# Kernel optimization log

Measured on AMD Instinct MI355X. Metric: run time of the kernel, lower is better.

Reference implementation:

```python
import jax, jax.numpy as jnp
import numpy as np

D_MODEL = 1024
N_HEADS = 16
D_HEAD = D_MODEL // N_HEADS
HIDDEN = 4 * D_MODEL
EPS = 1e-5
ROPE_BASE = 10000.0


def layernorm(x, g, b):
    mu = jnp.mean(x, axis=-1, keepdims=True)
    var = jnp.mean((x - mu) ** 2, axis=-1, keepdims=True)
    return (x - mu) * jax.lax.rsqrt(var + EPS) * g + b


def rope(t, pos):
    # t: (B, N, D), pos: (N,) int -> rotary transform over D (half-split pairs)
    half = t.shape[-1] // 2
    inv_freq = 1.0 / (ROPE_BASE ** (jnp.arange(half, dtype=jnp.float32) / half))
    ang = pos.astype(jnp.float32)[:, None] * inv_freq  # (N, half)
    cos, sin = jnp.cos(ang), jnp.sin(ang)
    t1, t2 = t[..., :half], t[..., half:]
    return jnp.concatenate([t1 * cos - t2 * sin, t1 * sin + t2 * cos], axis=-1)


def setup_inputs() -> dict:
    key = jax.random.key(0)
    ks = jax.random.split(key, 12)
    B, N, D, H = 2, 2048, D_MODEL, HIDDEN
    s = 0.02
    return {
        "x": jax.random.normal(ks[0], (B, N, D), jnp.float32),
        "pos": jnp.arange(N, dtype=jnp.int32),
        "Wq": jax.random.normal(ks[1], (D, D), jnp.float32) * s,
        "bq": jnp.zeros((D,), jnp.float32),
        "Wk": jax.random.normal(ks[2], (D, D), jnp.float32) * s,
        "bk": jnp.zeros((D,), jnp.float32),
        "Wv": jax.random.normal(ks[3], (D, D), jnp.float32) * s,
        "bv": jnp.zeros((D,), jnp.float32),
        "Wo": jax.random.normal(ks[4], (D, D), jnp.float32) * s,
        "bo": jnp.zeros((D,), jnp.float32),
        "g1": jnp.ones((D,), jnp.float32),
        "b1": jnp.zeros((D,), jnp.float32),
        "g2": jnp.ones((D,), jnp.float32),
        "b2": jnp.zeros((D,), jnp.float32),
        "W1": jax.random.normal(ks[5], (D, H), jnp.float32) * s,
        "bm1": jnp.zeros((H,), jnp.float32),
        "W2": jax.random.normal(ks[6], (H, D), jnp.float32) * s,
        "bm2": jnp.zeros((D,), jnp.float32),
    }


def reference(x, pos, Wq, bq, Wk, bk, Wv, bv, Wo, bo, g1, b1, g2, b2, W1, bm1, W2, bm2):
    B, N, D = x.shape
    Hh, dh = N_HEADS, D_HEAD

    # --- attention sublayer (pre-norm) ---
    h = layernorm(x, g1, b1)
    q = h @ Wq + bq
    k = h @ Wk + bk
    v = h @ Wv + bv
    q = rope(q, pos)
    k = rope(k, pos)
    # split heads: (B, Hh, N, dh)
    q = q.reshape(B, N, Hh, dh).transpose(0, 2, 1, 3)
    k = k.reshape(B, N, Hh, dh).transpose(0, 2, 1, 3)
    v = v.reshape(B, N, Hh, dh).transpose(0, 2, 1, 3)
    scores = jnp.einsum("bhqd,bhkd->bhqk", q, k) / jnp.sqrt(jnp.float32(dh))
    attn = jax.nn.softmax(scores, axis=-1)
    ctx = jnp.einsum("bhqk,bhkd->bhqd", attn, v)
    ctx = ctx.transpose(0, 2, 1, 3).reshape(B, N, D)
    x = x + ctx @ Wo + bo

    # --- MLP sublayer (pre-norm, exact GELU) ---
    h = layernorm(x, g2, b2)
    h = jax.nn.gelu(h @ W1 + bm1, approximate=False)
    x = x + h @ W2 + bm2
    return x
```

## Files before the change

### kernel.cpp

```cpp
#include <hip/hip_runtime.h>

typedef __bf16 bf16x8 __attribute__((ext_vector_type(8)));
typedef __bf16 bf16x4 __attribute__((ext_vector_type(4)));
typedef float  f32x4  __attribute__((ext_vector_type(4)));

#define D_MODEL 1024
#define SEQ     2048
#define BATCH   2
#define NH      16
#define DH      64
#define HID     4096
#define ROWS    (BATCH*SEQ)

static __device__ __forceinline__ void gl_lds16(const __bf16* g, __bf16* l) {
  __builtin_amdgcn_global_load_lds(
      (const __attribute__((address_space(1))) unsigned int*)g,
      (__attribute__((address_space(3))) unsigned int*)l, 16, 0, 0);
}

__global__ __launch_bounds__(256) void ln_kernel(
    const float* __restrict__ x, const float* __restrict__ g,
    const float* __restrict__ b, __bf16* __restrict__ out)
{
  int row = blockIdx.x;
  const float* xr = x + (size_t)row * D_MODEL;
  int i0 = threadIdx.x * 4;
  f32x4 xv = *(const f32x4*)(xr + i0);
  float s  = xv[0] + xv[1] + xv[2] + xv[3];
  float ss = xv[0]*xv[0] + xv[1]*xv[1] + xv[2]*xv[2] + xv[3]*xv[3];
#pragma unroll
  for (int off = 1; off < 64; off <<= 1) {
    s  += __shfl_xor(s,  off, 64);
    ss += __shfl_xor(ss, off, 64);
  }
  __shared__ float red[8];
  int wave = threadIdx.x >> 6;
  if ((threadIdx.x & 63) == 0) { red[wave] = s; red[4 + wave] = ss; }
  __syncthreads();
  s  = red[0] + red[1] + red[2] + red[3];
  ss = red[4] + red[5] + red[6] + red[7];
  float mu  = s * (1.0f / D_MODEL);
  float var = ss * (1.0f / D_MODEL) - mu * mu;
  float inv = rsqrtf(var + 1e-5f);
  f32x4 gv = *(const f32x4*)(g + i0);
  f32x4 bv = *(const f32x4*)(b + i0);
  bf16x4 ov;
#pragma unroll
  for (int j = 0; j < 4; ++j)
    ov[j] = (__bf16)((xv[j] - mu) * inv * gv[j] + bv[j]);
  *(bf16x4*)(out + (size_t)row * D_MODEL + i0) = ov;
}

__global__ __launch_bounds__(256) void convT_kernel(
    const float* __restrict__ W, __bf16* __restrict__ Wt, int K, int N)
{
  __shared__ float T[32][33];
  int n0 = blockIdx.x * 32, k0 = blockIdx.y * 32;
  int r  = threadIdx.x >> 3;
  int c4 = (threadIdx.x & 7) * 4;
  f32x4 v = *(const f32x4*)(W + (size_t)(k0 + r) * N + n0 + c4);
#pragma unroll
  for (int i = 0; i < 4; ++i) T[r][c4 + i] = v[i];
  __syncthreads();
  bf16x4 o;
#pragma unroll
  for (int i = 0; i < 4; ++i) o[i] = (__bf16)T[c4 + i][r];
  *(bf16x4*)(Wt + (size_t)(n0 + r) * K + k0 + c4) = o;
}

__global__ void biascat_kernel(const float* __restrict__ a,
                               const float* __restrict__ b,
                               const float* __restrict__ c,
                               float* __restrict__ o)
{
  int i = blockIdx.x * 256 + threadIdx.x;
  o[i] = i < 1024 ? a[i] : (i < 2048 ? b[i - 1024] : c[i - 2048]);
}

__global__ __launch_bounds__(512, 2) void gemm256(
    const __bf16* __restrict__ A, const __bf16* __restrict__ Bt,
    const float* __restrict__ bias, const float* __restrict__ resid,
    void* __restrict__ Cv, int M, int N, int K, int act, int c_fp32)
{
  __shared__ __bf16 As[2][256 * 64];
  __shared__ __bf16 Bs[2][256 * 64];
  int tid = threadIdx.x, lane = tid & 63, wv = tid >> 6;
  int quad = lane >> 4, l16 = lane & 15;
  int wr = wv >> 2, wc = wv & 3;
  int gx = M >> 8, gy = N >> 8;
  int nwg = gx * gy;
  int xcd = blockIdx.x & 7;
  int q = nwg >> 3, r8 = nwg & 7;
  int wg = (xcd < r8 ? xcd * (q + 1) : r8 * (q + 1) + (xcd - r8) * q) + (blockIdx.x >> 3);
  int row0 = (wg % gx) << 8;
  int col0 = (wg / gx) << 8;
  int s_r  = lane >> 3;
  int s_src = ((lane & 7) ^ s_r) * 8;
  int sw = l16 & 7;
  int NT = K >> 6;
  f32x4 acc[8][4] = {};

#define G256_STAGE(kt, b)                                                     \
  {                                                                           \
    int k0_ = (kt) * 64;                                                      \
    _Pragma("unroll")                                                         \
    for (int rd = 0; rd < 4; ++rd) {                                          \
      int rrow = rd * 64 + wv * 8 + s_r;                                      \
      gl_lds16(A  + (size_t)(row0 + rrow) * K + k0_ + s_src,                  \
               &As[b][rd * 4096 + wv * 512]);                                 \
      gl_lds16(Bt + (size_t)(col0 + rrow) * K + k0_ + s_src,                  \
               &Bs[b][rd * 4096 + wv * 512]);                                 \
    }                                                                         \
  }

  G256_STAGE(0, 0);
  G256_STAGE(1, 1);

  for (int t = 0; t < NT; ++t) {
    if (t + 1 < NT) asm volatile("s_waitcnt vmcnt(8)" ::: "memory");
    else            asm volatile("s_waitcnt vmcnt(0)" ::: "memory");
    __builtin_amdgcn_s_barrier();
    const __bf16* Ab = &As[t & 1][0];
    const __bf16* Bb = &Bs[t & 1][0];
    __builtin_amdgcn_s_setprio(1);
#pragma unroll
    for (int kk = 0; kk < 2; ++kk) {
      int slot = ((kk * 4 + quad) ^ sw) * 8;
      bf16x8 bfr[4];
#pragma unroll
      for (int j = 0; j < 4; ++j)
        bfr[j] = *(const bf16x8*)(Bb + (wc * 64 + j * 16 + l16) * 64 + slot);
      bf16x8 afr[8];
#pragma unroll
      for (int i = 0; i < 8; ++i)
        afr[i] = *(const bf16x8*)(Ab + (wr * 128 + i * 16 + l16) * 64 + slot);
#pragma unroll
      for (int i = 0; i < 8; ++i)
#pragma unroll
        for (int j = 0; j < 4; ++j)
          acc[i][j] = __builtin_amdgcn_mfma_f32_16x16x32_bf16(afr[i], bfr[j], acc[i][j], 0, 0, 0);
    }
    __builtin_amdgcn_s_setprio(0);
    __builtin_amdgcn_s_barrier();
    if (t + 2 < NT) G256_STAGE(t + 2, t & 1);
  }

#pragma unroll
  for (int i = 0; i < 8; ++i) {
    int grow = row0 + wr * 128 + i * 16 + quad * 4;
#pragma unroll
    for (int j = 0; j < 4; ++j) {
      int gcol = col0 + wc * 64 + j * 16 + l16;
      float bsv = bias[gcol];
#pragma unroll
      for (int r = 0; r < 4; ++r) {
        size_t off = (size_t)(grow + r) * N + gcol;
        float v = acc[i][j][r] + bsv;
        if (act) v = 0.5f * v * (1.0f + erff(v * 0.70710678118654752f));
        if (resid) v += resid[off];
        if (c_fp32) ((float*)Cv)[off] = v;
        else        ((__bf16*)Cv)[off] = (__bf16)v;
      }
    }
  }
}

__global__ __launch_bounds__(256) void gemm128(
    const __bf16* __restrict__ A, const __bf16* __restrict__ Bt,
    const float* __restrict__ bias, const float* __restrict__ resid,
    void* __restrict__ Cv, int M, int N, int K, int act, int c_fp32)
{
  __shared__ __bf16 As[128 * 64];
  __shared__ __bf16 Bs[128 * 64];
  int tid = threadIdx.x, lane = tid & 63, wv = tid >> 6;
  int quad = lane >> 4, l16 = lane & 15;
  int wr = wv >> 1, wc = wv & 1;
  int gx = M >> 7, gy = N >> 7;
  int blk = blockIdx.x;
  int xcd = blk & 7, t = blk >> 3;
  int row0 = (t % gx) * 128;
  int col0 = (xcd * (gy >> 3) + t / gx) * 128;
  int s_r8 = lane >> 3;
  int s_c8 = lane & 7;
  int s_src = (s_c8 ^ s_r8) * 8;
  int sw = l16 & 7;
  f32x4 acc[4][4] = {};

  for (int k0 = 0; k0 < K; k0 += 64) {
#pragma unroll
    for (int p = 0; p < 4; ++p) {
      int r = p * 32 + wv * 8 + s_r8;
      gl_lds16(A  + (size_t)(row0 + r) * K + k0 + s_src, As + p * 2048 + wv * 512);
      gl_lds16(Bt + (size_t)(col0 + r) * K + k0 + s_src, Bs + p * 2048 + wv * 512);
    }
    __syncthreads();
#pragma unroll
    for (int kk = 0; kk < 2; ++kk) {
      int slot = ((kk * 4 + quad) ^ sw) * 8;
      bf16x8 af[4], bf[4];
#pragma unroll
      for (int i = 0; i < 4; ++i) {
        af[i] = *(const bf16x8*)(As + (wr * 64 + i * 16 + l16) * 64 + slot);
        bf[i] = *(const bf16x8*)(Bs + (wc * 64 + i * 16 + l16) * 64 + slot);
      }
#pragma unroll
      for (int i = 0; i < 4; ++i)
#pragma unroll
        for (int j = 0; j < 4; ++j)
          acc[i][j] = __builtin_amdgcn_mfma_f32_16x16x32_bf16(af[i], bf[j], acc[i][j], 0, 0, 0);
    }
    __syncthreads();
  }
#pragma unroll
  for (int i = 0; i < 4; ++i) {
    int grow = row0 + wr * 64 + i * 16 + quad * 4;
#pragma unroll
    for (int j = 0; j < 4; ++j) {
      int gcol = col0 + wc * 64 + j * 16 + l16;
      float bsv = bias[gcol];
#pragma unroll
      for (int r = 0; r < 4; ++r) {
        size_t off = (size_t)(grow + r) * N + gcol;
        float v = acc[i][j][r] + bsv;
        if (act) v = 0.5f * v * (1.0f + erff(v * 0.70710678118654752f));
        if (resid) v += resid[off];
        if (c_fp32) ((float*)Cv)[off] = v;
        else        ((__bf16*)Cv)[off] = (__bf16)v;
      }
    }
  }
}

__global__ __launch_bounds__(256) void gemm64x128(
    const __bf16* __restrict__ A, const __bf16* __restrict__ Bt,
    const float* __restrict__ bias, const float* __restrict__ resid,
    void* __restrict__ Cv, int M, int N, int K, int act, int c_fp32)
{
  __shared__ __bf16 As[2][64 * 64];
  __shared__ __bf16 Bs[2][128 * 64];
  int tid = threadIdx.x, lane = tid & 63, wv = tid >> 6;
  int quad = lane >> 4, l16 = lane & 15;
  int wr = wv >> 1, wc = wv & 1;
  int gx = M >> 6, gy = N >> 7;
  int blk = blockIdx.x;
  int xcd = blk & 7, t = blk >> 3;
  int row0 = (t % gx) * 64;
  int col0 = (xcd * (gy >> 3) + t / gx) * 128;
  int s_r8 = lane >> 3;
  int s_c8 = lane & 7;
  int s_src = (s_c8 ^ s_r8) * 8;
  int sw = l16 & 7;
  int NT = K >> 6;
  f32x4 acc[2][4] = {};

#define G64_STAGE(kt, b)                                                      \
  {                                                                           \
    int k0_ = (kt) * 64;                                                      \
    _Pragma("unroll")                                                         \
    for (int p = 0; p < 4; ++p) {                                             \
      int r = p * 32 + wv * 8 + s_r8;                                         \
      if (p < 2)                                                              \
        gl_lds16(A + (size_t)(row0 + r) * K + k0_ + s_src,                    \
                 &As[b][p * 2048 + wv * 512]);                                \
      gl_lds16(Bt + (size_t)(col0 + r) * K + k0_ + s_src,                     \
               &Bs[b][p * 2048 + wv * 512]);                                  \
    }                                                                         \
  }

  G64_STAGE(0, 0);
  G64_STAGE(1, 1);

  for (int tt = 0; tt < NT; ++tt) {
    if (tt + 1 < NT) asm volatile("s_waitcnt vmcnt(6)" ::: "memory");
    else             asm volatile("s_waitcnt vmcnt(0)" ::: "memory");
    __builtin_amdgcn_s_barrier();
    const __bf16* Ab = &As[tt & 1][0];
    const __bf16* Bb = &Bs[tt & 1][0];
    __builtin_amdgcn_s_setprio(1);
#pragma unroll
    for (int kk = 0; kk < 2; ++kk) {
      int slot = ((kk * 4 + quad) ^ sw) * 8;
      bf16x8 af[2], bf[4];
#pragma unroll
      for (int i = 0; i < 2; ++i)
        af[i] = *(const bf16x8*)(Ab + (wr * 32 + i * 16 + l16) * 64 + slot);
#pragma unroll
      for (int j = 0; j < 4; ++j)
        bf[j] = *(const bf16x8*)(Bb + (wc * 64 + j * 16 + l16) * 64 + slot);
#pragma unroll
      for (int i = 0; i < 2; ++i)
#pragma unroll
        for (int j = 0; j < 4; ++j)
          acc[i][j] = __builtin_amdgcn_mfma_f32_16x16x32_bf16(af[i], bf[j], acc[i][j], 0, 0, 0);
    }
    __builtin_amdgcn_s_setprio(0);
    __builtin_amdgcn_s_barrier();
    if (tt + 2 < NT) G64_STAGE(tt + 2, tt & 1);
  }

#pragma unroll
  for (int i = 0; i < 2; ++i) {
    int grow = row0 + wr * 32 + i * 16 + quad * 4;
#pragma unroll
    for (int j = 0; j < 4; ++j) {
      int gcol = col0 + wc * 64 + j * 16 + l16;
      float bsv = bias[gcol];
#pragma unroll
      for (int r = 0; r < 4; ++r) {
        size_t off = (size_t)(grow + r) * N + gcol;
        float v = acc[i][j][r] + bsv;
        if (act) v = 0.5f * v * (1.0f + erff(v * 0.70710678118654752f));
        if (resid) v += resid[off];
        if (c_fp32) ((float*)Cv)[off] = v;
        else        ((__bf16*)Cv)[off] = (__bf16)v;
      }
    }
  }
}

__global__ __launch_bounds__(256) void rope_repack(
    const __bf16* __restrict__ qkv, const int* __restrict__ pos,
    __bf16* __restrict__ Qh, __bf16* __restrict__ Kh)
{
  int row = blockIdx.x;
  int b = row >> 11, n = row & (SEQ - 1);
  float p = (float)pos[n];
  const __bf16* qr = qkv + (size_t)row * 3072;
#pragma unroll
  for (int t = 0; t < 2; ++t) {
    int i = threadIdx.x + t * 256;
    float fr  = expf(-9.210340371976184f * ((float)i * (1.0f / 512.0f)));
    float ang = p * fr;
    float sn, c;
    sincosf(ang, &sn, &c);
    float q1 = (float)qr[i],        q2 = (float)qr[512 + i];
    float k1 = (float)qr[1024 + i], k2 = (float)qr[1536 + i];
    int h1 = i >> 6, d1 = i & 63;
    int h2 = (i + 512) >> 6;
    size_t o1 = ((size_t)(b * NH + h1) * SEQ + n) * DH + d1;
    size_t o2 = ((size_t)(b * NH + h2) * SEQ + n) * DH + d1;
    Qh[o1] = (__bf16)((q1 * c - q2 * sn) * 0.125f);
    Qh[o2] = (__bf16)((q1 * sn + q2 * c) * 0.125f);
    Kh[o1] = (__bf16)(k1 * c - k2 * sn);
    Kh[o2] = (__bf16)(k1 * sn + k2 * c);
  }
}

__global__ __launch_bounds__(256) void vtrans_kernel(
    const __bf16* __restrict__ Vsrc, int vstride, __bf16* __restrict__ Vt,
    int blocked)
{
  __shared__ __bf16 T[64][72];
  int bh = blockIdx.x;
  int kb = blockIdx.y * 64;
  int b = bh >> 4, h = bh & 15;
  int tid = threadIdx.x;
#pragma unroll
  for (int t = 0; t < 2; ++t) {
    int u = tid + t * 256;
    int r = u >> 3, seg = (u & 7) * 8;
    bf16x8 v = *(const bf16x8*)(Vsrc + (size_t)(b * SEQ + kb + r) * vstride + h * DH + seg);
    *(bf16x8*)(&T[r][seg]) = v;
  }
  __syncthreads();
#pragma unroll
  for (int t = 0; t < 2; ++t) {
    int u = tid + t * 256;
    int d = u >> 3, ks = (u & 7) * 8;
    bf16x8 o;
#pragma unroll
    for (int i = 0; i < 8; ++i) o[i] = T[ks + i][d];
    if (blocked) {
      int key = kb + ks;
      *(bf16x8*)(Vt + (((size_t)bh * (SEQ / 128) + (key >> 7)) * DH + d) * 128 + (key & 127)) = o;
    } else {
      *(bf16x8*)(Vt + ((size_t)bh * DH + d) * SEQ + kb + ks) = o;
    }
  }
}

#define KS 136
__global__ __launch_bounds__(256) void attn_split(
    const __bf16* __restrict__ Qh, const __bf16* __restrict__ Kh,
    const __bf16* __restrict__ Vt, __bf16* __restrict__ pacc,
    float* __restrict__ pml)
{
  __shared__ __bf16 Ks[128 * 64];
  __shared__ __bf16 Vs[64 * 128];
  __shared__ __bf16 Pl[4][16 * KS];
  int tid = threadIdx.x, lane = tid & 63, wave = tid >> 6;
  int quad = lane >> 4, l16 = lane & 15;
  int blk = blockIdx.x;
  int split = blk >> 10;
  int rr = blk & 1023;
  int bh  = ((rr & 7) << 2) | ((rr >> 3) & 3);
  int q64 = rr >> 5;
  int q0 = q64 * 64 + wave * 16;
  const __bf16* qbase = Qh + (size_t)bh * SEQ * DH;
  const __bf16* kbase = Kh + (size_t)bh * SEQ * DH;
  const __bf16* vbase = Vt + (size_t)bh * SEQ * DH;
  const __bf16* qp = qbase + (size_t)(q0 + l16) * DH + quad * 8;
  bf16x8 qf0 = *(const bf16x8*)(qp);
  bf16x8 qf1 = *(const bf16x8*)(qp + 32);
  float lrow[4] = {0.f, 0.f, 0.f, 0.f};
  f32x4 acc[4] = {};
  __bf16* pw = &Pl[wave][0];
  int s_kr = lane >> 3;
  int s_k8 = lane & 7;
  int s_vd = lane >> 4;
  int s_vs = lane & 15;
  int sw8  = l16 & 7;

  int kb0 = split * (SEQ / 2);
  for (int it = 0; it < (SEQ / 2) / 128; ++it) {
    int kb = kb0 + it * 128;
    const __bf16* kt = kbase + (size_t)kb * DH;
    const __bf16* vt = vbase + (size_t)(kb >> 7) * (DH * 128);
    __syncthreads();
#pragma unroll
    for (int p = 0; p < 4; ++p) {
      int key0 = p * 32 + wave * 8;
      int swz  = (key0 >> 3) & 7;
      gl_lds16(kt + (key0 + s_kr) * DH + ((s_k8 ^ swz) * 8), Ks + p * 2048 + wave * 512);
      int d = p * 16 + wave * 4 + s_vd;
      gl_lds16(vt + d * 128 + ((s_vs ^ (d & 15)) * 8), Vs + p * 2048 + wave * 512);
    }
    __syncthreads();
    f32x4 s[8];
#pragma unroll
    for (int j = 0; j < 8; ++j) {
      const __bf16* kr = Ks + (l16 * 8 + j) * 64;
      bf16x8 kf0 = *(const bf16x8*)(kr + (quad ^ sw8) * 8);
      bf16x8 kf1 = *(const bf16x8*)(kr + ((quad ^ sw8) ^ 4) * 8);
      f32x4 z = {};
      z = __builtin_amdgcn_mfma_f32_16x16x32_bf16(qf0, kf0, z, 0, 0, 0);
      s[j] = __builtin_amdgcn_mfma_f32_16x16x32_bf16(qf1, kf1, z, 0, 0, 0);
    }
#pragma unroll
    for (int r = 0; r < 4; ++r) {
      bf16x8 pv;
      float rs = 0.f;
#pragma unroll
      for (int j = 0; j < 8; ++j) {
        float pj = __expf(s[j][r]);
        rs += pj;
        pv[j] = (__bf16)pj;
      }
      lrow[r] += rs;
      *(bf16x8*)(pw + (quad * 4 + r) * KS + l16 * 8) = pv;
    }
#pragma unroll
    for (int kk = 0; kk < 4; ++kk) {
      bf16x8 pf = *(const bf16x8*)(pw + l16 * KS + kk * 32 + quad * 8);
#pragma unroll
      for (int j = 0; j < 4; ++j) {
        int d = j * 16 + l16;
        bf16x8 vf = *(const bf16x8*)(Vs + d * 128 + (((kk * 4 + quad) ^ (d & 15)) * 8));
        acc[j] = __builtin_amdgcn_mfma_f32_16x16x32_bf16(pf, vf, acc[j], 0, 0, 0);
      }
    }
  }
#pragma unroll
  for (int r = 0; r < 4; ++r)
#pragma unroll
    for (int off = 1; off < 16; off <<= 1) lrow[r] += __shfl_xor(lrow[r], off, 64);
#pragma unroll
  for (int r = 0; r < 4; ++r) {
    int brow = wave * 16 + quad * 4 + r;
#pragma unroll
    for (int j = 0; j < 4; ++j)
      pacc[((size_t)blk * 64 + brow) * 64 + j * 16 + l16] = (__bf16)acc[j][r];
    if (l16 == 0) {
      pml[(size_t)blk * 128 + brow]      = 0.f;
      pml[(size_t)blk * 128 + 64 + brow] = lrow[r];
    }
  }
}

__global__ __launch_bounds__(256) void attn_combine(
    const __bf16* __restrict__ pacc, const float* __restrict__ pml,
    __bf16* __restrict__ ctx)
{
  int bq = blockIdx.x;
  int q64 = bq & 31, bh = bq >> 5;
  int b = bh >> 4, h = bh & 15;
  int tid = threadIdx.x;
  int r = tid >> 2;
  int c = (tid & 3) * 16;
  int blk0 = ((q64 * 4 + (bh & 3)) << 3) | (bh >> 2);
  int blk1 = blk0 + 1024;
  float m0 = pml[(size_t)blk0 * 128 + r], l0 = pml[(size_t)blk0 * 128 + 64 + r];
  float m1 = pml[(size_t)blk1 * 128 + r], l1 = pml[(size_t)blk1 * 128 + 64 + r];
  float m = fmaxf(m0, m1);
  float w0 = __expf(m0 - m), w1 = __expf(m1 - m);
  float inv = 1.0f / (w0 * l0 + w1 * l1);
  size_t r0 = ((size_t)blk0 * 64 + r) * 64 + c;
  size_t r1 = ((size_t)blk1 * 64 + r) * 64 + c;
  size_t ob = ((size_t)(b * SEQ) + q64 * 64 + r) * D_MODEL + h * DH + c;
#pragma unroll
  for (int g = 0; g < 2; ++g) {
    bf16x8 a0 = *(const bf16x8*)(pacc + r0 + g * 8);
    bf16x8 a1 = *(const bf16x8*)(pacc + r1 + g * 8);
    bf16x8 o;
#pragma unroll
    for (int i = 0; i < 8; ++i)
      o[i] = (__bf16)((w0 * (float)a0[i] + w1 * (float)a1[i]) * inv);
    *(bf16x8*)(ctx + ob + g * 8) = o;
  }
}

__global__ __launch_bounds__(256) void rope_inplace(
    __bf16* __restrict__ ql, __bf16* __restrict__ kl,
    const int* __restrict__ pos, int stride)
{
  int row = blockIdx.x;
  int n = row & (SEQ - 1);
  float p = (float)pos[n];
  const size_t rbase = (size_t)row * stride;
#pragma unroll
  for (int t = 0; t < 2; ++t) {
    int i = threadIdx.x + t * 256;
    float fr  = expf(-9.210340371976184f * ((float)i * (1.0f / 512.0f)));
    float ang = p * fr;
    float sn, c;
    sincosf(ang, &sn, &c);
    float q1 = (float)ql[rbase + i], q2 = (float)ql[rbase + 512 + i];
    float k1 = (float)kl[rbase + i], k2 = (float)kl[rbase + 512 + i];
    ql[rbase + i]       = (__bf16)(q1 * c - q2 * sn);
    ql[rbase + 512 + i] = (__bf16)(q1 * sn + q2 * c);
    kl[rbase + i]       = (__bf16)(k1 * c - k2 * sn);
    kl[rbase + 512 + i] = (__bf16)(k1 * sn + k2 * c);
  }
}

__global__ __launch_bounds__(256) void attn_kernel(
    const __bf16* __restrict__ Q, const __bf16* __restrict__ K,
    const __bf16* __restrict__ Vt, __bf16* __restrict__ ctx, int qkstride)
{
  __shared__ __bf16 Pl[4][16 * KS];
  int tid = threadIdx.x, lane = tid & 63, wave = tid >> 6;
  int quad = lane >> 4, l16 = lane & 15;
  int blk = blockIdx.x;
  int q64 = blk & 31;
  int bh  = blk >> 5;
  int b = bh >> 4, h = bh & 15;
  int q0 = q64 * 64 + wave * 16;
  const __bf16* qbase = Q + (size_t)b * SEQ * qkstride + h * DH;
  const __bf16* kbase = K + (size_t)b * SEQ * qkstride + h * DH;
  const __bf16* vbase = Vt + (size_t)bh * DH * SEQ;
  const __bf16* qp = qbase + (size_t)(q0 + l16) * qkstride + quad * 8;
  bf16x8 qf0 = *(const bf16x8*)(qp);
  bf16x8 qf1 = *(const bf16x8*)(qp + 32);
  float mrow[4] = {-1e30f, -1e30f, -1e30f, -1e30f};
  float lrow[4] = {0.f, 0.f, 0.f, 0.f};
  f32x4 acc[4] = {};
  __bf16* pw = &Pl[wave][0];

  for (int kb = 0; kb < SEQ; kb += 128) {
    f32x4 s[8];
#pragma unroll
    for (int j = 0; j < 8; ++j) {
      const __bf16* kp = kbase + (size_t)(kb + l16 * 8 + j) * qkstride + quad * 8;
      bf16x8 kf0 = *(const bf16x8*)(kp);
      bf16x8 kf1 = *(const bf16x8*)(kp + 32);
      f32x4 z = {};
      z = __builtin_amdgcn_mfma_f32_16x16x32_bf16(qf0, kf0, z, 0, 0, 0);
      z = __builtin_amdgcn_mfma_f32_16x16x32_bf16(qf1, kf1, z, 0, 0, 0);
#pragma unroll
      for (int r = 0; r < 4; ++r) s[j][r] = z[r] * 0.125f;
    }
#pragma unroll
    for (int r = 0; r < 4; ++r) {
      float mx = s[0][r];
#pragma unroll
      for (int j = 1; j < 8; ++j) mx = fmaxf(mx, s[j][r]);
#pragma unroll
      for (int off = 1; off < 16; off <<= 1) mx = fmaxf(mx, __shfl_xor(mx, off, 64));
      float mn = fmaxf(mrow[r], mx);
      float al = __expf(mrow[r] - mn);
      float p[8], rs = 0.f;
#pragma unroll
      for (int j = 0; j < 8; ++j) { p[j] = __expf(s[j][r] - mn); rs += p[j]; }
#pragma unroll
      for (int off = 1; off < 16; off <<= 1) rs += __shfl_xor(rs, off, 64);
      lrow[r] = lrow[r] * al + rs;
      mrow[r] = mn;
#pragma unroll
      for (int j = 0; j < 4; ++j) acc[j][r] *= al;
      bf16x8 pv;
#pragma unroll
      for (int j = 0; j < 8; ++j) pv[j] = (__bf16)p[j];
      *(bf16x8*)(pw + (quad * 4 + r) * KS + l16 * 8) = pv;
    }
#pragma unroll
    for (int kk = 0; kk < 4; ++kk) {
      bf16x8 pf = *(const bf16x8*)(pw + l16 * KS + kk * 32 + quad * 8);
#pragma unroll
      for (int j = 0; j < 4; ++j) {
        bf16x8 vf = *(const bf16x8*)(vbase + (size_t)(j * 16 + l16) * SEQ + kb + kk * 32 + quad * 8);
        acc[j] = __builtin_amdgcn_mfma_f32_16x16x32_bf16(pf, vf, acc[j], 0, 0, 0);
      }
    }
  }
#pragma unroll
  for (int r = 0; r < 4; ++r) {
    int row = q0 + quad * 4 + r;
    float inv = 1.0f / lrow[r];
    size_t obase = ((size_t)(b * SEQ) + row) * D_MODEL + h * DH;
#pragma unroll
    for (int j = 0; j < 4; ++j)
      ctx[obase + j * 16 + l16] = (__bf16)(acc[j][r] * inv);
  }
}

extern "C" void kernel_launch(void* const* d_in, const int* in_sizes, int n_in,
                              void* d_out, int out_size, void* d_ws, size_t ws_size,
                              hipStream_t stream)
{
  const float* x   = (const float*)d_in[0];
  const int*   pos = (const int*)  d_in[1];
  const float* Wq  = (const float*)d_in[2];
  const float* bq  = (const float*)d_in[3];
  const float* Wk  = (const float*)d_in[4];
  const float* bk  = (const float*)d_in[5];
  const float* Wv  = (const float*)d_in[6];
  const float* bv  = (const float*)d_in[7];
  const float* Wo  = (const float*)d_in[8];
  const float* bo  = (const float*)d_in[9];
  const float* g1  = (const float*)d_in[10];
  const float* b1  = (const float*)d_in[11];
  const float* g2  = (const float*)d_in[12];
  const float* b2  = (const float*)d_in[13];
  const float* W1  = (const float*)d_in[14];
  const float* bm1 = (const float*)d_in[15];
  const float* W2  = (const float*)d_in[16];
  const float* bm2 = (const float*)d_in[17];
  float* out = (float*)d_out;

  const size_t MB = 1024 * 1024;
  char* w = (char*)d_ws;
  dim3 blk(256);
  dim3 blk512(512);
  dim3 gConvD(D_MODEL / 32, D_MODEL / 32);
  dim3 gConv1(HID / 32, D_MODEL / 32);
  dim3 gConv2(D_MODEL / 32, HID / 32);
  dim3 gVt(BATCH * NH, SEQ / 64);

  if (ws_size >= (size_t)96 * MB) {
    __bf16* hln   = (__bf16*)(w + 0 * MB);
    float*  x1    = (float*) (w + 8 * MB);
    __bf16* qkv   = (__bf16*)(w + 24 * MB);
    __bf16* pacc  = (__bf16*)(w + 24 * MB);
    float*  pml   = (float*) (w + 41 * MB);
    __bf16* hmlp  = (__bf16*)(w + 24 * MB);
    __bf16* Qh    = (__bf16*)(w + 48 * MB);
    __bf16* ctx   = (__bf16*)(w + 48 * MB);
    __bf16* Kh    = (__bf16*)(w + 56 * MB);
    __bf16* W2T   = (__bf16*)(w + 56 * MB);
    __bf16* Vt    = (__bf16*)(w + 64 * MB);
    __bf16* W1T   = (__bf16*)(w + 64 * MB);
    __bf16* WqkvT = (__bf16*)(w + 72 * MB);
    __bf16* WoT   = (__bf16*)(w + 78 * MB);
    float*  bqkv  = (float*) (w + 80 * MB);

    convT_kernel<<<gConvD, blk, 0, stream>>>(Wq, WqkvT,               D_MODEL, D_MODEL);
    convT_kernel<<<gConvD, blk, 0, stream>>>(Wk, WqkvT + 1024 * 1024, D_MODEL, D_MODEL);
    convT_kernel<<<gConvD, blk, 0, stream>>>(Wv, WqkvT + 2048 * 1024, D_MODEL, D_MODEL);
    convT_kernel<<<gConvD, blk, 0, stream>>>(Wo, WoT, D_MODEL, D_MODEL);
    biascat_kernel<<<12, blk, 0, stream>>>(bq, bk, bv, bqkv);
    ln_kernel<<<ROWS, blk, 0, stream>>>(x, g1, b1, hln);
    gemm256<<<(ROWS / 256) * (3072 / 256), blk512, 0, stream>>>(hln, WqkvT, bqkv, nullptr, qkv, ROWS, 3072, D_MODEL, 0, 0);
    rope_repack<<<ROWS, blk, 0, stream>>>(qkv, pos, Qh, Kh);
    vtrans_kernel<<<gVt, blk, 0, stream>>>(qkv + 2048, 3072, Vt, 1);
    attn_split<<<BATCH * NH * (SEQ / 64) * 2, blk, 0, stream>>>(Qh, Kh, Vt, pacc, pml);
    attn_combine<<<BATCH * NH * (SEQ / 64), blk, 0, stream>>>(pacc, pml, ctx);
    convT_kernel<<<gConv1, blk, 0, stream>>>(W1, W1T, D_MODEL, HID);
    convT_kernel<<<gConv2, blk, 0, stream>>>(W2, W2T, HID, D_MODEL);
    gemm64x128<<<(ROWS / 64) * (D_MODEL / 128), blk, 0, stream>>>(ctx, WoT, bo, x, x1, ROWS, D_MODEL, D_MODEL, 0, 1);
    ln_kernel<<<ROWS, blk, 0, stream>>>(x1, g2, b2, hln);
    gemm256<<<(ROWS / 256) * (HID / 256), blk512, 0, stream>>>(hln, W1T, bm1, nullptr, hmlp, ROWS, HID, D_MODEL, 1, 0);
    gemm64x128<<<(ROWS / 64) * (D_MODEL / 128), blk, 0, stream>>>(hmlp, W2T, bm2, x1, out, ROWS, D_MODEL, HID, 0, 1);
  } else {
    __bf16* hln  = (__bf16*)(w + 0 * MB);
    __bf16* vlin = (__bf16*)(w + 8 * MB);
    __bf16* WqT  = (__bf16*)(w + 16 * MB);
    __bf16* WkT  = (__bf16*)(w + 18 * MB);
    __bf16* WvT  = (__bf16*)(w + 20 * MB);
    __bf16* ctx  = (__bf16*)(w + 16 * MB);
    __bf16* WoT  = (__bf16*)(w + 8 * MB);
    __bf16* W1T  = (__bf16*)(w + 8 * MB);
    __bf16* W2T  = (__bf16*)(w + 16 * MB);
    __bf16* Vt   = (__bf16*)(w + 24 * MB);
    __bf16* hmlp = (__bf16*)(w + 24 * MB);
    __bf16* qlin = (__bf16*)d_out;
    __bf16* klin = (__bf16*)d_out + (size_t)ROWS * D_MODEL;
    float*  x1   = (float*)d_out;

    convT_kernel<<<gConvD, blk, 0, stream>>>(Wq, WqT, D_MODEL, D_MODEL);
    convT_kernel<<<gConvD, blk, 0, stream>>>(Wk, WkT, D_MODEL, D_MODEL);
    convT_kernel<<<gConvD, blk, 0, stream>>>(Wv, WvT, D_MODEL, D_MODEL);
    ln_kernel<<<ROWS, blk, 0, stream>>>(x, g1, b1, hln);
    int nLin = (ROWS / 64) * (D_MODEL / 128);
    gemm64x128<<<nLin, blk, 0, stream>>>(hln, WqT, bq, nullptr, qlin, ROWS, D_MODEL, D_MODEL, 0, 0);
    gemm64x128<<<nLin, blk, 0, stream>>>(hln, WkT, bk, nullptr, klin, ROWS, D_MODEL, D_MODEL, 0, 0);
    gemm64x128<<<nLin, blk, 0, stream>>>(hln, WvT, bv, nullptr, vlin, ROWS, D_MODEL, D_MODEL, 0, 0);
    rope_inplace<<<ROWS, blk, 0, stream>>>(qlin, klin, pos, D_MODEL);
    vtrans_kernel<<<gVt, blk, 0, stream>>>(vlin, D_MODEL, Vt, 0);
    attn_kernel<<<BATCH * NH * (SEQ / 64), blk, 0, stream>>>(qlin, klin, Vt, ctx, D_MODEL);
    convT_kernel<<<gConvD, blk, 0, stream>>>(Wo, WoT, D_MODEL, D_MODEL);
    gemm64x128<<<nLin, blk, 0, stream>>>(ctx, WoT, bo, x, x1, ROWS, D_MODEL, D_MODEL, 0, 1);
    ln_kernel<<<ROWS, blk, 0, stream>>>(x1, g2, b2, hln);
    convT_kernel<<<gConv1, blk, 0, stream>>>(W1, W1T, D_MODEL, HID);
    convT_kernel<<<gConv2, blk, 0, stream>>>(W2, W2T, HID, D_MODEL);
    const int CH = 1024;
    for (int c = 0; c < ROWS / CH; ++c) {
      const __bf16* a1 = hln + (size_t)c * CH * D_MODEL;
      gemm128<<<(CH / 128) * (HID / 128), blk, 0, stream>>>(a1, W1T, bm1, nullptr, hmlp, CH, HID, D_MODEL, 1, 0);
      gemm64x128<<<(CH / 64) * (D_MODEL / 128), blk, 0, stream>>>(hmlp, W2T, bm2, x1 + (size_t)c * CH * D_MODEL,
                                          out + (size_t)c * CH * D_MODEL, CH, D_MODEL, HID, 0, 1);
    }
  }
}
```

Baseline: 428.2 us.

## Double-buffer K/V tiles in split attention with async prefetch and exp2 softmax

```diff
diff --git a/kernel.cpp b/kernel.cpp
--- a/kernel.cpp
+++ b/kernel.cpp
@@ -326,6 +326,7 @@
   int b = row >> 11, n = row & (SEQ - 1);
   float p = (float)pos[n];
   const __bf16* qr = qkv + (size_t)row * 3072;
+  const float QS = 0.125f * 1.44269504088896f;
 #pragma unroll
   for (int t = 0; t < 2; ++t) {
     int i = threadIdx.x + t * 256;
@@ -339,8 +340,8 @@
     int h2 = (i + 512) >> 6;
     size_t o1 = ((size_t)(b * NH + h1) * SEQ + n) * DH + d1;
     size_t o2 = ((size_t)(b * NH + h2) * SEQ + n) * DH + d1;
-    Qh[o1] = (__bf16)((q1 * c - q2 * sn) * 0.125f);
-    Qh[o2] = (__bf16)((q1 * sn + q2 * c) * 0.125f);
+    Qh[o1] = (__bf16)((q1 * c - q2 * sn) * QS);
+    Qh[o2] = (__bf16)((q1 * sn + q2 * c) * QS);
     Kh[o1] = (__bf16)(k1 * c - k2 * sn);
     Kh[o2] = (__bf16)(k1 * sn + k2 * c);
   }
@@ -385,9 +386,9 @@
     const __bf16* __restrict__ Vt, __bf16* __restrict__ pacc,
     float* __restrict__ pml)
 {
-  __shared__ __bf16 Ks[128 * 64];
-  __shared__ __bf16 Vs[64 * 128];
-  __shared__ __bf16 Pl[4][16 * KS];
+  __shared__ __bf16 Ks[2][128 * 64];
+  __shared__ __bf16 Vs[2][64 * 128];
+  __shared__ __bf16 Pl[4][16 * 128];
   int tid = threadIdx.x, lane = tid & 63, wave = tid >> 6;
   int quad = lane >> 4, l16 = lane & 15;
   int blk = blockIdx.x;
@@ -410,55 +411,75 @@
   int s_vd = lane >> 4;
   int s_vs = lane & 15;
   int sw8  = l16 & 7;
-
   int kb0 = split * (SEQ / 2);
-  for (int it = 0; it < (SEQ / 2) / 128; ++it) {
-    int kb = kb0 + it * 128;
-    const __bf16* kt = kbase + (size_t)kb * DH;
-    const __bf16* vt = vbase + (size_t)(kb >> 7) * (DH * 128);
-    __syncthreads();
-#pragma unroll
-    for (int p = 0; p < 4; ++p) {
-      int key0 = p * 32 + wave * 8;
-      int swz  = (key0 >> 3) & 7;
-      gl_lds16(kt + (key0 + s_kr) * DH + ((s_k8 ^ swz) * 8), Ks + p * 2048 + wave * 512);
-      int d = p * 16 + wave * 4 + s_vd;
-      gl_lds16(vt + d * 128 + ((s_vs ^ (d & 15)) * 8), Vs + p * 2048 + wave * 512);
-    }
-    __syncthreads();
+  const int NT = (SEQ / 2) / 128;
+
+#define ATTN_STAGE(it_, b_)                                                   \
+  {                                                                           \
+    int kb_ = kb0 + (it_) * 128;                                              \
+    const __bf16* kt_ = kbase + (size_t)kb_ * DH;                             \
+    const __bf16* vt_ = vbase + (size_t)(kb_ >> 7) * (DH * 128);              \
+    _Pragma("unroll")                                                         \
+    for (int p = 0; p < 4; ++p) {                                             \
+      int key0 = p * 32 + wave * 8;                                           \
+      int swz  = (key0 >> 3) & 7;                                             \
+      gl_lds16(kt_ + (key0 + s_kr) * DH + ((s_k8 ^ swz) * 8),                 \
+               &Ks[b_][p * 2048 + wave * 512]);                               \
+      int d = p * 16 + wave * 4 + s_vd;                                       \
+      gl_lds16(vt_ + d * 128 + ((s_vs ^ (d & 15)) * 8),                       \
+               &Vs[b_][p * 2048 + wave * 512]);                               \
+    }                                                                         \
+  }
+
+  ATTN_STAGE(0, 0);
+  ATTN_STAGE(1, 1);
+
+  for (int it = 0; it < NT; ++it) {
+    if (it + 1 < NT) asm volatile("s_waitcnt vmcnt(8)" ::: "memory");
+    else             asm volatile("s_waitcnt vmcnt(0)" ::: "memory");
+    __builtin_amdgcn_s_barrier();
+    const __bf16* Kb = &Ks[it & 1][0];
+    const __bf16* Vb = &Vs[it & 1][0];
     f32x4 s[8];
+    __builtin_amdgcn_s_setprio(1);
 #pragma unroll
     for (int j = 0; j < 8; ++j) {
-      const __bf16* kr = Ks + (l16 * 8 + j) * 64;
+      const __bf16* kr = Kb + (l16 * 8 + j) * 64;
       bf16x8 kf0 = *(const bf16x8*)(kr + (quad ^ sw8) * 8);
       bf16x8 kf1 = *(const bf16x8*)(kr + ((quad ^ sw8) ^ 4) * 8);
       f32x4 z = {};
       z = __builtin_amdgcn_mfma_f32_16x16x32_bf16(qf0, kf0, z, 0, 0, 0);
       s[j] = __builtin_amdgcn_mfma_f32_16x16x32_bf16(qf1, kf1, z, 0, 0, 0);
     }
+    __builtin_amdgcn_s_setprio(0);
 #pragma unroll
     for (int r = 0; r < 4; ++r) {
+      int ro = quad * 4 + r;
       bf16x8 pv;
       float rs = 0.f;
 #pragma unroll
       for (int j = 0; j < 8; ++j) {
-        float pj = __expf(s[j][r]);
+        float pj = exp2f(s[j][r]);
         rs += pj;
         pv[j] = (__bf16)pj;
       }
       lrow[r] += rs;
-      *(bf16x8*)(pw + (quad * 4 + r) * KS + l16 * 8) = pv;
-    }
+      *(bf16x8*)(pw + ro * 128 + ((l16 ^ ro) * 8)) = pv;
+    }
+    __builtin_amdgcn_s_setprio(1);
 #pragma unroll
     for (int kk = 0; kk < 4; ++kk) {
-      bf16x8 pf = *(const bf16x8*)(pw + l16 * KS + kk * 32 + quad * 8);
+      bf16x8 pf = *(const bf16x8*)(pw + l16 * 128 + (((kk * 4 + quad) ^ l16) * 8));
 #pragma unroll
       for (int j = 0; j < 4; ++j) {
         int d = j * 16 + l16;
-        bf16x8 vf = *(const bf16x8*)(Vs + d * 128 + (((kk * 4 + quad) ^ (d & 15)) * 8));
+        bf16x8 vf = *(const bf16x8*)(Vb + d * 128 + (((kk * 4 + quad) ^ (d & 15)) * 8));
         acc[j] = __builtin_amdgcn_mfma_f32_16x16x32_bf16(pf, vf, acc[j], 0, 0, 0);
       }
     }
+    __builtin_amdgcn_s_setprio(0);
+    __builtin_amdgcn_s_barrier();
+    if (it + 2 < NT) ATTN_STAGE(it + 2, it & 1);
   }
 #pragma unroll
   for (int r = 0; r < 4; ++r)
```

Measured after the change: 485.0 us (median of 2 runs). 1.13x slower.
